# Performance work log

Hardware: AMD Instinct MI355X
Metric: run time of the kernel (lower is better)

The kernel has to match this reference:

```python
import math
import jax, jax.numpy as jnp
import numpy as np

B, HRV, WRV, CRV = 1, 32, 512, 64
CBEV, HB, WB = 128, 256, 256
D, COUT, K, HEADS, P = 128, 128, 5, 8, 6
HD = D // HEADS
NBINS = 110
RMAX, BIN = 55.0, 0.5
XMIN, XMAX, YMIN, YMAX = -55.0, 55.0, -55.0, 55.0

_ELEV = np.array([-30.67, -29.33, -28.0, -26.66, -25.33, -24.0, -22.67, -21.33,
                  -20.0, -18.67, -17.33, -16.0, -14.67, -13.33, -12.0, -10.67,
                  -9.33, -8.0, -6.66, -5.33, -4.0, -2.67, -1.33, 0.0, 1.33,
                  2.67, 4.0, 5.33, 6.67, 8.0, 9.33, 10.67], dtype=np.float32)

def _make_uvec():
    az_line = np.linspace(-math.pi, math.pi, WRV + 1, dtype=np.float32)[:-1]
    az = az_line + 0.5 * (az_line[1] - az_line[0])
    elev = np.deg2rad(_ELEV[::-1].reshape(HRV, -1).mean(axis=1)).astype(np.float32)
    az2 = np.broadcast_to(az[None, :], (HRV, WRV))
    el2 = np.broadcast_to(elev[:, None], (HRV, WRV))
    ux = np.cos(az2) * np.cos(el2)
    uy = np.sin(az2) * np.cos(el2)
    uz = np.broadcast_to(np.sin(el2), (HRV, WRV))
    return jnp.asarray(ux), jnp.asarray(uy), jnp.asarray(uz)

_UX, _UY, _UZ = _make_uvec()

def _lin(x, w, b):
    # 1x1 conv / Linear: w is torch-layout [Cout, Cin]
    return jnp.einsum('...c,oc->...o', x, w) + b

def _gn(x, gamma, beta, groups, eps=1e-5):
    Bn, H, W, C = x.shape
    xg = x.reshape(Bn, H, W, groups, C // groups)
    mu = xg.mean(axis=(1, 2, 4), keepdims=True)
    var = ((xg - mu) ** 2).mean(axis=(1, 2, 4), keepdims=True)
    xg = (xg - mu) * jax.lax.rsqrt(var + eps)
    return xg.reshape(Bn, H, W, C) * gamma + beta

def _gelu(x):
    return jax.nn.gelu(x, approximate=False)

def _conv3x3_circ(x, w):
    # torch Conv2d(3x3, padding=1, padding_mode='circular', bias=False)
    xp = jnp.pad(x, ((0, 0), (1, 1), (1, 1), (0, 0)), mode='wrap')
    k = jnp.transpose(w, (2, 3, 1, 0))  # OIHW -> HWIO
    return jax.lax.conv_general_dilated(xp, k, (1, 1), 'VALID',
                                        dimension_numbers=('NHWC', 'HWIO', 'NHWC'))

def _deform_sample(v, loc, aw):
    # v: [B, HB*WB, HEADS, HD]; loc: [B,Nq,HEADS,P,2] normalized; aw: [B,Nq,HEADS,P]
    # Emulates grid_sample(bilinear, zeros padding, align_corners=False).
    Bq = v.shape[0]
    vflat = jnp.transpose(v, (0, 2, 1, 3))       # [B, H, HW, hd]
    loc_t = jnp.transpose(loc, (0, 2, 1, 3, 4))  # [B, H, Nq, P, 2]
    aw_t = jnp.transpose(aw, (0, 2, 1, 3))       # [B, H, Nq, P]
    x = loc_t[..., 0] * WB - 0.5
    y = loc_t[..., 1] * HB - 0.5
    x0 = jnp.floor(x); y0 = jnp.floor(y)
    wx1 = x - x0; wy1 = y - y0
    x0i = x0.astype(jnp.int32); y0i = y0.astype(jnp.int32)
    gather = jax.vmap(jax.vmap(lambda vf, idx: vf[idx]))  # over B, heads
    def corner(xi, yi, wgt, acc):
        valid = (xi >= 0) & (xi < WB) & (yi >= 0) & (yi < HB)
        idx = jnp.clip(yi, 0, HB - 1) * WB + jnp.clip(xi, 0, WB - 1)
        g = gather(vflat, idx)  # [B, H, Nq, P, hd]
        return acc + g * (wgt * valid.astype(g.dtype))[..., None]
    acc = jnp.zeros(x.shape + (HD,), dtype=v.dtype)
    acc = corner(x0i,     y0i,     (1 - wx1) * (1 - wy1), acc)
    acc = corner(x0i + 1, y0i,     wx1 * (1 - wy1), acc)
    acc = corner(x0i,     y0i + 1, (1 - wx1) * wy1, acc)
    acc = corner(x0i + 1, y0i + 1, wx1 * wy1, acc)
    out = (acc * aw_t[..., None]).sum(axis=3)    # [B, H, Nq, hd]
    return jnp.transpose(out, (0, 2, 1, 3)).reshape(Bq, -1, D)

def _forward(x_rv, bev, lidar2ego_mat, wq, bq, wv, bv, wo, bo,
             qd_w1, qd_b1, qd_w2, qd_b2,
             rh_w1, rh_b1, rh_g1, rh_be1, rh_w2, rh_g2, rh_be2, rh_w3, rh_b3,
             off_w, off_b, aw_w, aw_b, vp_w, vp_b, op_w, op_b):
    Bq = x_rv.shape[0]
    Q0 = _lin(x_rv, wq, bq)                                   # [B,Hrv,Wrv,D]
    Vmap = _lin(jnp.transpose(bev, (0, 2, 3, 1)), wv, bv)     # [B,HB,WB,D]
    uvec = jnp.broadcast_to(jnp.stack([_UX, _UY, _UZ], axis=-1)[None], (Bq, HRV, WRV, 3))
    h = _gelu(_gn(_lin(jnp.concatenate([x_rv, uvec], axis=-1), rh_w1, rh_b1), rh_g1, rh_be1, 8))
    h = _gelu(_gn(_conv3x3_circ(h, rh_w2), rh_g2, rh_be2, 8))
    depth_logits = _lin(h, rh_w3, rh_b3)                      # [B,Hrv,Wrv,NBINS]
    depth_dist = jax.nn.softmax(depth_logits, axis=-1)
    topk_prob, topk_idx = jax.lax.top_k(depth_dist, K)        # [B,Hrv,Wrv,K]
    topk_depths = jnp.minimum(BIN * (topk_idx.astype(jnp.float32) + 0.5), RMAX - 0.5 * BIN)
    xl = topk_depths * _UX[None, :, :, None]
    yl = topk_depths * _UY[None, :, :, None]
    zl = topk_depths * _UZ[None, :, :, None]
    p = jnp.stack([xl, yl, zl, jnp.ones_like(xl)], axis=-1)   # [B,Hrv,Wrv,K,4]
    pe = jnp.einsum('bhwki,ij->bhwkj', p, lidar2ego_mat[0])
    rx = (pe[..., 0] - XMIN) / (XMAX - XMIN)
    ry = (pe[..., 1] - YMIN) / (YMAX - YMIN)
    ref_pts = jnp.stack([jnp.clip(rx, 0.0, 1.0), jnp.clip(ry, 0.0, 1.0)], axis=-1).reshape(Bq, -1, 2)
    qin = jnp.concatenate([jnp.broadcast_to(Q0[:, :, :, None, :], (Bq, HRV, WRV, K, D)),
                           (topk_depths / RMAX)[..., None]], axis=-1)
    query = _lin(_gelu(_lin(qin, qd_w1, qd_b1)), qd_w2, qd_b2).reshape(Bq, -1, D)
    value = Vmap.reshape(Bq, -1, D)
    # --- MSDA (mmcv MultiScaleDeformableAttention, 1 level) ---
    v = _lin(value, vp_w, vp_b).reshape(Bq, -1, HEADS, HD)
    Nq = query.shape[1]
    off = _lin(query, off_w, off_b).reshape(Bq, Nq, HEADS, P, 2)
    aw = jax.nn.softmax(_lin(query, aw_w, aw_b).reshape(Bq, Nq, HEADS, P), axis=-1)
    loc = ref_pts[:, :, None, None, :] + off / jnp.array([WB, HB], dtype=jnp.float32)
    y_msda = _lin(_deform_sample(v, loc, aw), op_w, op_b) + query  # residual add
    y_msda = y_msda.reshape(Bq, HRV, WRV, K, D)
    wgt = topk_prob / (topk_prob.sum(axis=-1, keepdims=True) + 1e-8)
    y = (y_msda * wgt[..., None]).sum(axis=3)
    y = _lin(y, wo, bo)                                       # [B,Hrv,Wrv,COUT]
    return y, jnp.transpose(depth_logits, (0, 3, 1, 2))

def setup_inputs():
    key = jax.random.key(0)
    ks = jax.random.split(key, 32)
    def rn(i, shape, s):
        return jax.random.normal(ks[i], shape, dtype=jnp.float32) * s
    return dict(
        x_rv=rn(0, (B, HRV, WRV, CRV), 1.0),
        bev=rn(1, (B, CBEV, HB, WB), 1.0),
        lidar2ego_mat=jnp.eye(4, dtype=jnp.float32)[None] + rn(2, (1, 4, 4), 0.01),
        wq=rn(3, (D, CRV), 0.05), bq=rn(4, (D,), 0.01),
        wv=rn(5, (D, CBEV), 0.05), bv=rn(6, (D,), 0.01),
        wo=rn(7, (COUT, D), 0.05), bo=rn(8, (COUT,), 0.01),
        qd_w1=rn(9, (D, D + 1), 0.05), qd_b1=rn(10, (D,), 0.01),
        qd_w2=rn(11, (D, D), 0.05), qd_b2=rn(12, (D,), 0.01),
        rh_w1=rn(13, (128, CRV + 3), 0.05), rh_b1=rn(14, (128,), 0.01),
        rh_g1=jnp.ones((128,), jnp.float32), rh_be1=jnp.zeros((128,), jnp.float32),
        rh_w2=rn(15, (64, 128, 3, 3), 0.05),
        rh_g2=jnp.ones((64,), jnp.float32), rh_be2=jnp.zeros((64,), jnp.float32),
        rh_w3=rn(16, (NBINS, 64), 0.05), rh_b3=rn(17, (NBINS,), 0.01),
        off_w=rn(18, (HEADS * P * 2, D), 0.02), off_b=rn(19, (HEADS * P * 2,), 2.0),
        aw_w=rn(20, (HEADS * P, D), 0.02), aw_b=rn(21, (HEADS * P,), 0.01),
        vp_w=rn(22, (D, D), 0.05), vp_b=rn(23, (D,), 0.01),
        op_w=rn(24, (D, D), 0.05), op_b=rn(25, (D,), 0.01),
    )

def reference(x_rv, bev, lidar2ego_mat, wq, bq, wv, bv, wo, bo,
              qd_w1, qd_b1, qd_w2, qd_b2,
              rh_w1, rh_b1, rh_g1, rh_be1, rh_w2, rh_g2, rh_be2, rh_w3, rh_b3,
              off_w, off_b, aw_w, aw_b, vp_w, vp_b, op_w, op_b):
    return _forward(x_rv, bev, lidar2ego_mat, wq, bq, wv, bv, wo, bo,
                    qd_w1, qd_b1, qd_w2, qd_b2,
                    rh_w1, rh_b1, rh_g1, rh_be1, rh_w2, rh_g2, rh_be2, rh_w3, rh_b3,
                    off_w, off_b, aw_w, aw_b, vp_w, vp_b, op_w, op_b)
```

## Files before the change

kernel.cpp:

```cpp
#include <hip/hip_runtime.h>
#include <math.h>

#define NT 256

typedef unsigned short u16;
typedef unsigned int u32;
typedef _Float16 f16;
typedef __attribute__((ext_vector_type(2))) unsigned int u32x2;
typedef __attribute__((ext_vector_type(4))) unsigned int u32x4;
typedef __attribute__((ext_vector_type(4))) float f32x4;
typedef __attribute__((ext_vector_type(8))) short s16x8;
typedef __attribute__((ext_vector_type(8))) _Float16 f16x8;

namespace {

__device__ const float c_elev[32] = {
  -30.67f,-29.33f,-28.0f,-26.66f,-25.33f,-24.0f,-22.67f,-21.33f,
  -20.0f,-18.67f,-17.33f,-16.0f,-14.67f,-13.33f,-12.0f,-10.67f,
  -9.33f,-8.0f,-6.66f,-5.33f,-4.0f,-2.67f,-1.33f,0.0f,1.33f,
  2.67f,4.0f,5.33f,6.67f,8.0f,9.33f,10.67f };

__device__ __forceinline__ float gelu_f(float x) {
  return 0.5f * x * (1.0f + erff(x * 0.70710678118654752440f));
}
__device__ __forceinline__ u16 bf16rne(float f) {
  u32 u = __builtin_bit_cast(u32, f);
  u32 r = u + 0x7FFFu + ((u >> 16) & 1u);
  return (u16)(r >> 16);
}
__device__ __forceinline__ float bf2f(u16 h) {
  u32 u = ((u32)h) << 16;
  return __builtin_bit_cast(float, u);
}
__device__ __forceinline__ float bflo(u32 v) {
  return __builtin_bit_cast(float, v << 16);
}
__device__ __forceinline__ float bfhi(u32 v) {
  return __builtin_bit_cast(float, v & 0xFFFF0000u);
}
__device__ __forceinline__ u32 packsplit(float x) {
  f16 h = (f16)x;
  f16 l = (f16)(x - (float)h);
  return (u32)__builtin_bit_cast(u16, h) | ((u32)__builtin_bit_cast(u16, l) << 16);
}
__device__ __forceinline__ void unpack16(u32x4 a, u32x4 b, f16x8& hi, f16x8& lo) {
  u32x4 h, l;
  h[0] = (a[0] & 0xFFFFu) | (a[1] << 16);  l[0] = (a[0] >> 16) | (a[1] & 0xFFFF0000u);
  h[1] = (a[2] & 0xFFFFu) | (a[3] << 16);  l[1] = (a[2] >> 16) | (a[3] & 0xFFFF0000u);
  h[2] = (b[0] & 0xFFFFu) | (b[1] << 16);  l[2] = (b[0] >> 16) | (b[1] & 0xFFFF0000u);
  h[3] = (b[2] & 0xFFFFu) | (b[3] << 16);  l[3] = (b[2] >> 16) | (b[3] & 0xFFFF0000u);
  hi = __builtin_bit_cast(f16x8, h);
  lo = __builtin_bit_cast(f16x8, l);
}

template<int COREAL, int CO, int KPAD, int CI, int PROD, int AMODE, bool DOGELU, bool OBF, bool GN = false>
__global__ __launch_bounds__(NT)
void slin(const float* __restrict__ Af, const float* __restrict__ A2,
          const u32* __restrict__ Wp, const float* __restrict__ bias,
          const float* __restrict__ gs, const float* __restrict__ gamma,
          const float* __restrict__ beta,
          float* __restrict__ outF, u16* __restrict__ outB)
{
  constexpr int BM = 64;
  constexpr int NFR = CO / 16;
  constexpr int KS = KPAD / 32;
  __shared__ u32 lds[BM * KPAD];
  const int tid = threadIdx.x;
  const long row0 = (long)blockIdx.x * BM;

  for (int i = tid; i < BM * (KPAD / 4); i += NT) {
    int r = i / (KPAD / 4), c = (i % (KPAD / 4)) * 4;
    long pix = row0 + r;
    u32x4 o;
    if constexpr (AMODE == 0) {
      if (c + 3 < CI) {
        f32x4 v = *(const f32x4*)(Af + pix * CI + c);
#pragma unroll
        for (int e = 0; e < 4; e++) {
          float x = v[e];
          if constexpr (GN) {
            int cc = c + e, g = cc >> 3;
            float mu = gs[2 * g] * (1.0f / 131072.0f);
            float var = gs[2 * g + 1] * (1.0f / 131072.0f) - mu * mu;
            x = (x - mu) * rsqrtf(var + 1e-5f) * gamma[cc] + beta[cc];
            x = gelu_f(x);
          }
          o[e] = packsplit(x);
        }
// ... 41 lines not shown
  for (int ks = 0; ks < KS; ks++) {
    const int arow = mb + lr;
    const u32 sw = (arow & 7) << 4;
    const int base = arow * KPAD * 4 + ks * 128 + kq * 32;
    u32x4 a0 = *(const u32x4*)((char*)lds + (base ^ sw));
    u32x4 a1 = *(const u32x4*)((char*)lds + ((base + 16) ^ sw));
    f16x8 ah, al;
    unpack16(a0, a1, ah, al);
#pragma unroll
    for (int nf = 0; nf < NFR; nf++) {
      const u32* wp = Wp + (nf * 16 + lr) * KPAD + ks * 32 + kq * 8;
      u32x4 w0 = *(const u32x4*)wp;
      u32x4 w1 = *(const u32x4*)(wp + 4);
      f16x8 wh, wl;
      unpack16(w0, w1, wh, wl);
      acc[nf] = __builtin_amdgcn_mfma_f32_16x16x32_f16(ah, wh, acc[nf], 0, 0, 0);
      if constexpr (PROD == 3) {
        acc[nf] = __builtin_amdgcn_mfma_f32_16x16x32_f16(ah, wl, acc[nf], 0, 0, 0);
        acc[nf] = __builtin_amdgcn_mfma_f32_16x16x32_f16(al, wh, acc[nf], 0, 0, 0);
      }
    }
  }

#pragma unroll
  for (int nf = 0; nf < NFR; nf++) {
    int col = nf * 16 + lr;
    if (col >= COREAL) continue;
    float bcol = bias[col];
#pragma unroll
    for (int r = 0; r < 4; r++) {
      long row = row0 + mb + kq * 4 + r;
      float val = acc[nf][r] + bcol;
      if constexpr (DOGELU) val = gelu_f(val);
      if constexpr (OBF) outB[row * COREAL + col] = bf16rne(val);
      else               outF[row * COREAL + col] = val;
    }
  }
}

__global__ __launch_bounds__(NT)
void conv_mfma(const float* __restrict__ X, const u32* __restrict__ Wc,
               const float* __restrict__ gs, const float* __restrict__ gamma,
               const float* __restrict__ beta, float* __restrict__ Y)
{
  __shared__ u32 lds[4 * 18 * 128];
  const int tid = threadIdx.x;
  const int bRow = (blockIdx.x >> 5) * 2;
  const int bCol = (blockIdx.x & 31) * 16;

  for (int i = tid; i < 4 * 18 * 32; i += NT) {
    int c4 = (i & 31) * 4;
    int col = (i >> 5) % 18;
    int row = i / (18 * 32);
    int gy = (bRow + row - 1 + 32) & 31;
    int gx = (bCol + col - 1 + 512) & 511;
    f32x4 v = *(const f32x4*)(X + ((long)gy * 512 + gx) * 128 + c4);
    u32x4 o;
#pragma unroll
    for (int e = 0; e < 4; e++) {
      int cc = c4 + e, g = cc >> 4;
      float mu = gs[2 * g] * (1.0f / 262144.0f);
      float var = gs[2 * g + 1] * (1.0f / 262144.0f) - mu * mu;
      float x = (v[e] - mu) * rsqrtf(var + 1e-5f) * gamma[cc] + beta[cc];
      o[e] = packsplit(gelu_f(x));
    }
    *(u32x4*)((char*)lds + ((((row * 18 + col) * 128 + c4) * 4) ^ ((col & 7) << 4))) = o;
  }
  __syncthreads();
// ... 102 lines not shown
    s16x8 af[MFR], bfr[NFR];
#pragma unroll
    for (int mf = 0; mf < MFR; mf++) {
      int r = mb + mf * 16 + lr;
      af[mf] = *(const s16x8*)(As + ((r * 256 + kof) ^ ((r & 7) << 4)));
    }
#pragma unroll
    for (int nf = 0; nf < NFR; nf++) {
      int r = nb + nf * 16 + lr;
      bfr[nf] = *(const s16x8*)(Bs + ((r * 256 + kof) ^ ((r & 7) << 4)));
    }
#pragma unroll
    for (int mf = 0; mf < MFR; mf++)
#pragma unroll
      for (int nf = 0; nf < NFR; nf++)
        acc[mf][nf] = __builtin_amdgcn_mfma_f32_16x16x32_bf16(af[mf], bfr[nf], acc[mf][nf], 0, 0, 0);
  }

#pragma unroll
  for (int mf = 0; mf < MFR; mf++) {
#pragma unroll
    for (int nf = 0; nf < NFR; nf++) {
      const int col = nb + nf * 16 + lr;
      const float bcol = bias[col];
      float ew = 0.f;
      if constexpr (DEPTH) ew = extraW[col];
#pragma unroll
      for (int r = 0; r < 4; r++) {
        long row = row0 + mb + mf * 16 + kq * 4 + r;
        float val = acc[mf][nf][r] + bcol;
        if constexpr (DEPTH) val += ew * (A2[row] * (1.0f / 55.0f));
        if constexpr (DOGELU) val = gelu_f(val);
        if constexpr (SPLIT) {
          if (col < 96) outF[row * 96 + col] = val;
          else if (col < 144) outB[row * 48 + (col - 96)] = bf16rne(val);
        } else {
          if constexpr (WF) outF[row * CO + col] = val;
          if constexpr (WBF) outB[row * CO + col] = bf16rne(val);
        }
      }
    }
  }
}

__global__ __launch_bounds__(NT)
void qmlp_kernel(const u16* __restrict__ Q0, const float* __restrict__ depths,
                 const u16* __restrict__ W1, const float* __restrict__ b1,
                 const float* __restrict__ w1last,
                 const u16* __restrict__ W2, const float* __restrict__ b2,
                 u16* __restrict__ query)
{
  __shared__ char smem[49152];
  char* As = smem;
  char* Bs = smem + 16384;
  const int tid = threadIdx.x;
  const long row0 = (long)blockIdx.x * 64;

  for (int i = tid; i < 128 * 16; i += NT) {
    int r = i >> 4, ck = i & 15;
    u32x4 v = ((const u32x4*)(W1 + r * 128))[ck];
    *(u32x4*)(Bs + ((r * 256 + ck * 16) ^ ((r & 7) << 4))) = v;
  }
  for (int i = tid; i < 64 * 16; i += NT) {
    int r = i >> 4, ck = i & 15;
    long src = (row0 + r) / 5;
    u32x4 v = ((const u32x4*)(Q0 + src * 128))[ck];
    *(u32x4*)(As + ((r * 256 + ck * 16) ^ ((r & 7) << 4))) = v;
// ... 166 lines not shown
                              const float* __restrict__ op_b, const float* __restrict__ bo,
                              u16* __restrict__ wc, float* __restrict__ bc,
                              u16* __restrict__ Wcat, float* __restrict__ cvec)
{
  int b = blockIdx.x, c = threadIdx.x;
  if (b < 128) {
    int o = b;
    float s = 0.f;
    for (int m = 0; m < 128; m++) s += vp_w[o * 128 + m] * wv[m * 128 + c];
    wc[o * 128 + c] = bf16rne(s);
    if (c == 0) {
      float bb = vp_b[o];
      for (int m = 0; m < 128; m++) bb += vp_w[o * 128 + m] * bv[m];
      bc[o] = bb;
    }
  } else {
    int o = b - 128;
    float s = 0.f;
    for (int m = 0; m < 128; m++) s += wo[o * 128 + m] * op_w[m * 128 + c];
    Wcat[o * 256 + c] = bf16rne(s);
    Wcat[o * 256 + 128 + c] = bf16rne(wo[o * 128 + c]);
    if (c == 0) {
      float bb = bo[o];
      for (int m = 0; m < 128; m++) bb += wo[o * 128 + m] * op_b[m];
      cvec[o] = bb;
    }
  }
}

__global__ void prepcvt_kernel(const float* __restrict__ qd_w1, const float* __restrict__ qd_w2,
                               const float* __restrict__ off_w, const float* __restrict__ aw_w,
                               const float* __restrict__ off_b, const float* __restrict__ aw_b,
                               const float* __restrict__ rh_w1, const float* __restrict__ rh_w3,
                               const float* __restrict__ wq, const float* __restrict__ rh_w2,
                               u16* Wq1, u16* Wq2, u16* Wmg, float* mgbias, float* w1last,
                               u32* Wh1, u32* Wlog, u32* Wq0, u32* Wcv, float* uvec)
{
  int i = blockIdx.x * NT + threadIdx.x;
  if (i < 16384) {
    int r = i >> 7, c = i & 127;
    Wq1[i] = bf16rne(qd_w1[r * 129 + c]);
    Wq2[i] = bf16rne(qd_w2[i]);
  }
  if (i < 20480) {
    int r = i >> 7, c = i & 127;
    float v = (r < 96) ? off_w[r * 128 + c] : ((r < 144) ? aw_w[(r - 96) * 128 + c] : 0.f);
    Wmg[i] = bf16rne(v);
  }
  if (i < 160) mgbias[i] = (i < 96) ? off_b[i] : ((i < 144) ? aw_b[i - 96] : 0.f);
  if (i < 128) w1last[i] = qd_w1[i * 129 + 128];
  if (i < 128 * 96) {
    int r = i / 96, c = i % 96;
    Wh1[i] = packsplit(c < 67 ? rh_w1[r * 67 + c] : 0.f);
  }
  if (i < 112 * 64) {
    int r = i / 64, c = i % 64;
    Wlog[i] = packsplit(r < 110 ? rh_w3[r * 64 + c] : 0.f);
  }
  if (i < 128 * 64) Wq0[i] = packsplit(wq[i]);
  if (i < 9 * 64 * 128) {
    int t = i / (64 * 128), o = (i / 128) % 64, c = i % 128;
    Wcv[i] = packsplit(rh_w2[(o * 128 + c) * 9 + t]);
  }
  if (i < 16384) {
    int hr = i >> 9, w = i & 511;
    float el = c_elev[31 - hr] * 0.017453292519943295f;
    float az = -3.14159265358979323846f + ((float)w + 0.5f) * (6.283185307179586477f / 512.0f);
    float ce = cosf(el);
    uvec[i * 3 + 0] = cosf(az) * ce;
    uvec[i * 3 + 1] = sinf(az) * ce;
    uvec[i * 3 + 2] = sinf(el);
  }
}

template<int C, int S>
__global__ __launch_bounds__(NT)
void gn_stats_kernel(const float* __restrict__ X, int Npix, float* __restrict__ gs)
{
  constexpr int PPB = NT / C;
  int tid = threadIdx.x;
  int c = tid % C;
  int psub = tid / C;
  float sum = 0.f, ss = 0.f;
  for (long pix = (long)blockIdx.x * PPB + psub; pix < Npix; pix += (long)gridDim.x * PPB) {
    float v = X[pix * C + c];
    sum += v; ss += v * v;
  }
  __shared__ float ls[8][2];
  if (tid < 16) ls[tid / 2][tid % 2] = 0.f;
  __syncthreads();
  int g = c / S;
  atomicAdd(&ls[g][0], sum);
  atomicAdd(&ls[g][1], ss);
  __syncthreads();
  if (tid < 16) atomicAdd(&gs[tid], ls[tid / 2][tid % 2]);
}

__global__ __launch_bounds__(NT)
void tlogits_kernel(const float* __restrict__ logits, float* __restrict__ out1)
{
  __shared__ float ls[128][111];
  int p0 = blockIdx.x * 128;
  for (int i = threadIdx.x; i < 128 * 110; i += NT) {
    int p = i / 110, c = i % 110;
    ls[p][c] = logits[(long)(p0 + p) * 110 + c];
  }
  __syncthreads();
  for (int i = threadIdx.x; i < 110 * 128; i += NT) {
    int c = i / 128, p = i % 128;
    out1[(long)c * 16384 + p0 + p] = ls[p][c];
  }
}

__global__ __launch_bounds__(NT)
void topk_kernel(const float* __restrict__ logits, float* __restrict__ depths,
                 float* __restrict__ wgt)
{
  int lane = threadIdx.x & 63;
  int pix = (blockIdx.x * NT + threadIdx.x) >> 6;
  const float* lr = logits + (long)pix * 110;
  float v0 = (lane < 110) ? lr[lane] : -1e30f;
  float v1 = (lane + 64 < 110) ? lr[lane + 64] : -1e30f;
  float m = fmaxf(v0, v1);
#pragma unroll
  for (int s = 32; s; s >>= 1) m = fmaxf(m, __shfl_xor(m, s));
  float ex = ((lane < 110) ? expf(v0 - m) : 0.f) + ((lane + 64 < 110) ? expf(v1 - m) : 0.f);
  float den = ex;
#pragma unroll
  for (int s = 32; s; s >>= 1) den += __shfl_xor(den, s);
  float pr[5]; int pi[5];
#pragma unroll
  for (int j = 0; j < 5; j++) {
    float bv; int bi;
    if (v0 >= v1) { bv = v0; bi = lane; } else { bv = v1; bi = lane + 64; }
    for (int s = 1; s < 64; s <<= 1) {
      float ov = __shfl_xor(bv, s);
      int oi = __shfl_xor(bi, s);
      if (ov > bv || (ov == bv && oi < bi)) { bv = ov; bi = oi; }
    }
    pr[j] = expf(bv - m) / den;
    pi[j] = bi;
    if (bi == lane) v0 = -1e30f;
    if (bi == lane + 64) v1 = -1e30f;
  }
  if (lane == 0) {
    float tot = pr[0] + pr[1] + pr[2] + pr[3] + pr[4] + 1e-8f;
#pragma unroll
    for (int j = 0; j < 5; j++) {
      depths[pix * 5 + j] = fminf(0.5f * ((float)pi[j] + 0.5f), 54.75f);
      wgt[pix * 5 + j] = pr[j] / tot;
    }
  }
}

__global__ __launch_bounds__(NT)
void msda_kernel(const u16* __restrict__ V, const float* __restrict__ depths,
                 const float* __restrict__ uvec, const float* __restrict__ L44,
                 const float* __restrict__ offb, const u16* __restrict__ awb,
                 u16* __restrict__ S)
{
  const int tid = threadIdx.x;
  const int kk = blockIdx.x >> 10;
  const int pg = blockIdx.x & 1023;
  const long pix = (long)pg * 16 + (tid >> 4);
  const int h = (tid >> 1) & 7;
  const int c0 = h * 16 + (tid & 1) * 8;
  const long q = pix * 5 + kk;

  float d = depths[q];
  float ux = uvec[pix * 3 + 0], uy = uvec[pix * 3 + 1], uz = uvec[pix * 3 + 2];
  float px = d * ux, py = d * uy, pz = d * uz;
  float pex = px * L44[0] + py * L44[4] + pz * L44[8] + L44[12];
  float pey = px * L44[1] + py * L44[5] + pz * L44[9] + L44[13];
  float rx = fminf(fmaxf((pex + 55.0f) * (1.0f / 110.0f), 0.f), 1.f);
  float ry = fminf(fmaxf((pey + 55.0f) * (1.0f / 110.0f), 0.f), 1.f);
  float rxs = rx * 256.0f - 0.5f;
  float rys = ry * 256.0f - 0.5f;

  const u32* ap32 = (const u32*)(awb + q * 48 + h * 6);
  u32 aw0 = ap32[0], aw1 = ap32[1], aw2 = ap32[2];
  float a[6] = { bflo(aw0), bfhi(aw0), bflo(aw1), bfhi(aw1), bflo(aw2), bfhi(aw2) };
  float mx = fmaxf(fmaxf(fmaxf(a[0], a[1]), fmaxf(a[2], a[3])), fmaxf(a[4], a[5]));
  float se = 0.f;
#pragma unroll
  for (int p = 0; p < 6; p++) { a[p] = __expf(a[p] - mx); se += a[p]; }
  const float inv = 1.0f / se;

  const f32x4* opv = (const f32x4*)(offb + q * 96 + h * 12);
  f32x4 of0 = opv[0], of1 = opv[1], of2 = opv[2];
  const float ox[6] = { of0[0], of0[2], of1[0], of1[2], of2[0], of2[2] };
  const float oy[6] = { of0[1], of0[3], of1[1], of1[3], of2[1], of2[3] };

  float acc[8];
#pragma unroll
  for (int j = 0; j < 8; j++) acc[j] = 0.f;

#pragma unroll
  for (int p = 0; p < 6; p++) {
    float x = rxs + ox[p];
    float y = rys + oy[p];
    float x0f = floorf(x), y0f = floorf(y);
    float wx = x - x0f, wy = y - y0f;
    int ix = (int)x0f, iy = (int)y0f;
    float awp = a[p] * inv;
    float wx0 = ((unsigned)ix < 256u) ? (1.f - wx) : 0.f;
    float wx1 = ((unsigned)(ix + 1) < 256u) ? wx : 0.f;
    float wy0 = ((unsigned)iy < 256u) ? (awp * (1.f - wy)) : 0.f;
    float wy1 = ((unsigned)(iy + 1) < 256u) ? (awp * wy) : 0.f;
    int xc0 = min(max(ix, 0), 255), xc1 = min(max(ix + 1, 0), 255);
    int yc0 = min(max(iy, 0), 255), yc1 = min(max(iy + 1, 0), 255);
#pragma unroll
    for (int cy = 0; cy < 2; cy++) {
      int yb = (cy ? yc1 : yc0) << 15;
      float wyv = cy ? wy1 : wy0;
#pragma unroll
      for (int cx = 0; cx < 2; cx++) {
        int idx = yb + ((cx ? xc1 : xc0) << 7) + c0;
        float m = (cx ? wx1 : wx0) * wyv;
        u32x4 v = *(const u32x4*)(V + idx);
#pragma unroll
        for (int e = 0; e < 4; e++) {
          acc[2 * e]     += m * bflo(v[e]);
          acc[2 * e + 1] += m * bfhi(v[e]);
        }
      }
    }
  }
  u32x4 o;
#pragma unroll
  for (int e = 0; e < 4; e++)
    o[e] = (u32)bf16rne(acc[2 * e]) | ((u32)bf16rne(acc[2 * e + 1]) << 16);
  *(u32x4*)(S + q * 128 + c0) = o;
}

}

extern "C" void kernel_launch(void* const* d_in, const int* in_sizes, int n_in,
                              void* d_out, int out_size, void* d_ws, size_t ws_size,
                              hipStream_t stream)
{
  (void)in_sizes; (void)n_in; (void)out_size; (void)ws_size;
  const float* x_rv   = (const float*)d_in[0];
  const float* bev    = (const float*)d_in[1];
  const float* L44    = (const float*)d_in[2];
  const float* wq     = (const float*)d_in[3];
  const float* bq     = (const float*)d_in[4];
  const float* wv     = (const float*)d_in[5];
  const float* bv     = (const float*)d_in[6];
  const float* woW    = (const float*)d_in[7];
  const float* boB    = (const float*)d_in[8];
  const float* qd_w1  = (const float*)d_in[9];
  const float* qd_b1  = (const float*)d_in[10];
  const float* qd_w2  = (const float*)d_in[11];
  const float* qd_b2  = (const float*)d_in[12];
  const float* rh_w1  = (const float*)d_in[13];
  const float* rh_b1  = (const float*)d_in[14];
  const float* rh_g1  = (const float*)d_in[15];
  const float* rh_be1 = (const float*)d_in[16];
  const float* rh_w2  = (const float*)d_in[17];
  const float* rh_g2  = (const float*)d_in[18];
  const float* rh_be2 = (const float*)d_in[19];
  const float* rh_w3  = (const float*)d_in[20];
  const float* rh_b3  = (const float*)d_in[21];
  const float* off_w  = (const float*)d_in[22];
  const float* off_b  = (const float*)d_in[23];
  const float* aw_w   = (const float*)d_in[24];
  const float* aw_b   = (const float*)d_in[25];
  const float* vp_w   = (const float*)d_in[26];
  const float* vp_b   = (const float*)d_in[27];
  const float* op_w   = (const float*)d_in[28];
  const float* op_b   = (const float*)d_in[29];

  float* outY = (float*)d_out;
  float* outL = (float*)d_out + 2097152;

  char* wsb = (char*)d_ws;
  size_t off = 0;
  auto alloc = [&](size_t bytes) -> char* {
    char* p = wsb + off;
    off += (bytes + 255) & ~(size_t)255;
    return p;
  };

  u16*   wcomb  = (u16*)alloc(32768);
  float* bcomb  = (float*)alloc(512);
  float* uvec   = (float*)alloc(196608);
  float* stats  = (float*)alloc(128);
  float* depths = (float*)alloc(327680);
  float* wgtb   = (float*)alloc(327680);
  float* w1last = (float*)alloc(512);
  u16*   Wq1    = (u16*)alloc(32768);
  u16*   Wq2    = (u16*)alloc(32768);
  u16*   Wmg    = (u16*)alloc(40960);
  float* mgbias = (float*)alloc(640);
  u16*   Wcat   = (u16*)alloc(65536);
  float* cvec   = (float*)alloc(512);
  u32*   Wh1    = (u32*)alloc(49152);
  u32*   Wlog   = (u32*)alloc(28672);
  u32*   Wq0    = (u32*)alloc(32768);
  u32*   Wcv    = (u32*)alloc(294912);
  char*  S1     = alloc(20971520);
  char*  S2     = alloc(4194304);
  char*  S3     = alloc(16777216);
  char*  S5     = alloc(20971520);
  float* offbuf = (float*)alloc(31457280);
  u16*   awbf   = (u16*)alloc(7864320);

  float* h1buf  = (float*)S1;
  float* logits = (float*)(S1 + 8388608);
  float* h2buf  = (float*)(S1 + 15597568);
  u16*   smp    = (u16*)S1;
  u16*   Q0bf   = (u16*)S2;
  u16*   vbuf   = (u16*)S3;
  u16*   querybf= (u16*)S5;

  float* stats1 = stats;
  float* stats2 = stats + 16;

  hipMemsetAsync((void*)stats, 0, 128, stream);

  prepmm_kernel<<<256, 128, 0, stream>>>(vp_w, wv, vp_b, bv, woW, op_w, op_b, boB,
                                         wcomb, bcomb, Wcat, cvec);
  prepcvt_kernel<<<288, NT, 0, stream>>>(qd_w1, qd_w2, off_w, aw_w, off_b, aw_b,
                                         rh_w1, rh_w3, wq, rh_w2,
                                         Wq1, Wq2, Wmg, mgbias, w1last,
                                         Wh1, Wlog, Wq0, Wcv, uvec);

  slin<128, 128, 64, 64, 1, 0, false, true><<<256, NT, 0, stream>>>(
      x_rv, nullptr, Wq0, bq, nullptr, nullptr, nullptr, nullptr, Q0bf);

  slin<128, 128, 96, 67, 3, 1, false, false><<<256, NT, 0, stream>>>(
      x_rv, uvec, Wh1, rh_b1, nullptr, nullptr, nullptr, h1buf, nullptr);
  gn_stats_kernel<128, 16><<<512, NT, 0, stream>>>(h1buf, 16384, stats1);
  conv_mfma<<<512, NT, 0, stream>>>(h1buf, Wcv, stats1, rh_g1, rh_be1, h2buf);
  gn_stats_kernel<64, 8><<<512, NT, 0, stream>>>(h2buf, 16384, stats2);
  slin<110, 112, 64, 64, 3, 0, false, false, true><<<256, NT, 0, stream>>>(
      h2buf, nullptr, Wlog, rh_b3, stats2, rh_g2, rh_be2, logits, nullptr);
  tlogits_kernel<<<128, NT, 0, stream>>>(logits, outL);
  topk_kernel<<<4096, NT, 0, stream>>>(logits, depths, wgtb);

  mfma_lin<128, 4, false, false, false, true, false><<<1024, NT, 0, stream>>>(
      bev, nullptr, wcomb, bcomb, nullptr, nullptr, vbuf, 65536);

  qmlp_kernel<<<1280, NT, 0, stream>>>(Q0bf, depths, Wq1, qd_b1, w1last, Wq2, qd_b2, querybf);

  mfma_lin<160, 0, false, false, false, false, true><<<1280, NT, 0, stream>>>(
      querybf, nullptr, Wmg, mgbias, nullptr, offbuf, awbf, 0);

  msda_kernel<<<5120, NT, 0, stream>>>(vbuf, depths, uvec, L44, offbuf, awbf, smp);

  outproj_kernel<<<256, NT, 0, stream>>>(smp, querybf, wgtb, Wcat, cvec, outY);
}
```

Baseline: 406.9 us.

## Store offsets as fp16, batch MSDA gathers, fuse logit transpose with top-k

The offset projection now writes sampling offsets as fp16 instead of fp32, halving that intermediate buffer, and the deformable sampler reads the packed halves. The sampler issues all 24 bilinear corner loads before accumulating, remaps block indices across 8 groups for locality, and sets a 3-blocks-per-SIMD launch bound. The logits transpose and softmax top-k are merged into one kernel that reads logits once from shared memory. The cost is fp16 rounding of offsets (offset bias is large, up to about 2), which slightly perturbs sample positions, plus higher register pressure from the batched loads.

```diff
diff --git a/kernel.cpp b/kernel.cpp
--- a/kernel.cpp
+++ b/kernel.cpp
@@ -331,7 +331,7 @@
         if constexpr (DEPTH) val += ew * (A2[row] * (1.0f / 55.0f));
         if constexpr (DOGELU) val = gelu_f(val);
         if constexpr (SPLIT) {
-          if (col < 96) outF[row * 96 + col] = val;
+          if (col < 96) ((u16*)outF)[row * 96 + col] = __builtin_bit_cast(u16, (f16)val);
           else if (col < 144) outB[row * 48 + (col - 96)] = bf16rne(val);
         } else {
           if constexpr (WF) outF[row * CO + col] = val;
@@ -629,71 +629,71 @@
 }
 
 __global__ __launch_bounds__(NT)
-void tlogits_kernel(const float* __restrict__ logits, float* __restrict__ out1)
-{
-  __shared__ float ls[128][111];
-  int p0 = blockIdx.x * 128;
-  for (int i = threadIdx.x; i < 128 * 110; i += NT) {
+void logpost_kernel(const float* __restrict__ logits, float* __restrict__ out1,
+                    float* __restrict__ depths, float* __restrict__ wgt)
+{
+  __shared__ float ls[64][112];
+  const int tid = threadIdx.x;
+  const int p0 = blockIdx.x * 64;
+  for (int i = tid; i < 64 * 110; i += NT) {
     int p = i / 110, c = i % 110;
     ls[p][c] = logits[(long)(p0 + p) * 110 + c];
   }
   __syncthreads();
-  for (int i = threadIdx.x; i < 110 * 128; i += NT) {
-    int c = i / 128, p = i % 128;
+  for (int i = tid; i < 110 * 64; i += NT) {
+    int c = i >> 6, p = i & 63;
     out1[(long)c * 16384 + p0 + p] = ls[p][c];
   }
-}
-
-__global__ __launch_bounds__(NT)
-void topk_kernel(const float* __restrict__ logits, float* __restrict__ depths,
-                 float* __restrict__ wgt)
-{
-  int lane = threadIdx.x & 63;
-  int pix = (blockIdx.x * NT + threadIdx.x) >> 6;
-  const float* lr = logits + (long)pix * 110;
-  float v0 = (lane < 110) ? lr[lane] : -1e30f;
-  float v1 = (lane + 64 < 110) ? lr[lane + 64] : -1e30f;
-  float m = fmaxf(v0, v1);
-#pragma unroll
-  for (int s = 32; s; s >>= 1) m = fmaxf(m, __shfl_xor(m, s));
-  float ex = ((lane < 110) ? expf(v0 - m) : 0.f) + ((lane + 64 < 110) ? expf(v1 - m) : 0.f);
-  float den = ex;
-#pragma unroll
-  for (int s = 32; s; s >>= 1) den += __shfl_xor(den, s);
-  float pr[5]; int pi[5];
-#pragma unroll
-  for (int j = 0; j < 5; j++) {
-    float bv; int bi;
-    if (v0 >= v1) { bv = v0; bi = lane; } else { bv = v1; bi = lane + 64; }
-    for (int s = 1; s < 64; s <<= 1) {
-      float ov = __shfl_xor(bv, s);
-      int oi = __shfl_xor(bi, s);
-      if (ov > bv || (ov == bv && oi < bi)) { bv = ov; bi = oi; }
-    }
-    pr[j] = expf(bv - m) / den;
-    pi[j] = bi;
-    if (bi == lane) v0 = -1e30f;
-    if (bi == lane + 64) v1 = -1e30f;
-  }
-  if (lane == 0) {
-    float tot = pr[0] + pr[1] + pr[2] + pr[3] + pr[4] + 1e-8f;
+  const int wave = tid >> 6, lane = tid & 63;
+  for (int t = 0; t < 16; t++) {
+    int p = wave * 16 + t;
+    float v0 = (lane < 110) ? ls[p][lane] : -1e30f;
+    float v1 = (lane + 64 < 110) ? ls[p][lane + 64] : -1e30f;
+    float m = fmaxf(v0, v1);
+#pragma unroll
+    for (int s = 32; s; s >>= 1) m = fmaxf(m, __shfl_xor(m, s));
+    float ex = ((lane < 110) ? expf(v0 - m) : 0.f) + ((lane + 64 < 110) ? expf(v1 - m) : 0.f);
+    float den = ex;
+#pragma unroll
+    for (int s = 32; s; s >>= 1) den += __shfl_xor(den, s);
+    float pr[5]; int pi[5];
 #pragma unroll
     for (int j = 0; j < 5; j++) {
-      depths[pix * 5 + j] = fminf(0.5f * ((float)pi[j] + 0.5f), 54.75f);
-      wgt[pix * 5 + j] = pr[j] / tot;
-    }
-  }
-}
-
-__global__ __launch_bounds__(NT)
+      float bv; int bi;
+      if (v0 >= v1) { bv = v0; bi = lane; } else { bv = v1; bi = lane + 64; }
+      for (int s = 1; s < 64; s <<= 1) {
+        float ov = __shfl_xor(bv, s);
+        int oi = __shfl_xor(bi, s);
+        if (ov > bv || (ov == bv && oi < bi)) { bv = ov; bi = oi; }
+      }
+      pr[j] = expf(bv - m) / den;
+      pi[j] = bi;
+      if (bi == lane) v0 = -1e30f;
+      if (bi == lane + 64) v1 = -1e30f;
+    }
+    if (lane == 0) {
+      long pix = p0 + p;
+      float tot = pr[0] + pr[1] + pr[2] + pr[3] + pr[4] + 1e-8f;
+#pragma unroll
+      for (int j = 0; j < 5; j++) {
+        depths[pix * 5 + j] = fminf(0.5f * ((float)pi[j] + 0.5f), 54.75f);
+        wgt[pix * 5 + j] = pr[j] / tot;
+      }
+    }
+  }
+}
+
+__global__ __launch_bounds__(NT, 3)
 void msda_kernel(const u16* __restrict__ V, const float* __restrict__ depths,
                  const float* __restrict__ uvec, const float* __restrict__ L44,
-                 const float* __restrict__ offb, const u16* __restrict__ awb,
+                 const u16* __restrict__ offH, const u16* __restrict__ awb,
                  u16* __restrict__ S)
 {
   const int tid = threadIdx.x;
-  const int kk = blockIdx.x >> 10;
-  const int pg = blockIdx.x & 1023;
+  const int hw = blockIdx.x;
+  const int bid = (hw & 7) * 640 + (hw >> 3);
+  const int kk = bid >> 10;
+  const int pg = bid & 1023;
   const long pix = (long)pg * 16 + (tid >> 4);
   const int h = (tid >> 1) & 7;
   const int c0 = h * 16 + (tid & 1) * 8;
@@ -718,19 +718,19 @@
   for (int p = 0; p < 6; p++) { a[p] = __expf(a[p] - mx); se += a[p]; }
   const float inv = 1.0f / se;
 
-  const f32x4* opv = (const f32x4*)(offb + q * 96 + h * 12);
-  f32x4 of0 = opv[0], of1 = opv[1], of2 = opv[2];
-  const float ox[6] = { of0[0], of0[2], of1[0], of1[2], of2[0], of2[2] };
-  const float oy[6] = { of0[1], of0[3], of1[1], of1[3], of2[1], of2[3] };
-
-  float acc[8];
-#pragma unroll
-  for (int j = 0; j < 8; j++) acc[j] = 0.f;
-
+  const u32* op16 = (const u32*)(offH + q * 96 + h * 12);
+  u32x2 o01 = *(const u32x2*)op16;
+  u32x2 o23 = *(const u32x2*)(op16 + 2);
+  u32x2 o45 = *(const u32x2*)(op16 + 4);
+  u32 ou[6] = { o01[0], o01[1], o23[0], o23[1], o45[0], o45[1] };
+
+  int ad[6][4]; float wt[6][4];
 #pragma unroll
   for (int p = 0; p < 6; p++) {
-    float x = rxs + ox[p];
-    float y = rys + oy[p];
+    float ox = (float)__builtin_bit_cast(f16, (u16)(ou[p] & 0xFFFFu));
+    float oy = (float)__builtin_bit_cast(f16, (u16)(ou[p] >> 16));
+    float x = rxs + ox;
+    float y = rys + oy;
     float x0f = floorf(x), y0f = floorf(y);
     float wx = x - x0f, wy = y - y0f;
     int ix = (int)x0f, iy = (int)y0f;
@@ -741,23 +741,31 @@
     float wy1 = ((unsigned)(iy + 1) < 256u) ? (awp * wy) : 0.f;
     int xc0 = min(max(ix, 0), 255), xc1 = min(max(ix + 1, 0), 255);
     int yc0 = min(max(iy, 0), 255), yc1 = min(max(iy + 1, 0), 255);
-#pragma unroll
-    for (int cy = 0; cy < 2; cy++) {
-      int yb = (cy ? yc1 : yc0) << 15;
-      float wyv = cy ? wy1 : wy0;
-#pragma unroll
-      for (int cx = 0; cx < 2; cx++) {
-        int idx = yb + ((cx ? xc1 : xc0) << 7) + c0;
-        float m = (cx ? wx1 : wx0) * wyv;
-        u32x4 v = *(const u32x4*)(V + idx);
-#pragma unroll
-        for (int e = 0; e < 4; e++) {
-          acc[2 * e]     += m * bflo(v[e]);
-          acc[2 * e + 1] += m * bfhi(v[e]);
-        }
-      }
-    }
-  }
+    ad[p][0] = (yc0 << 15) + (xc0 << 7) + c0;  wt[p][0] = wx0 * wy0;
+    ad[p][1] = (yc0 << 15) + (xc1 << 7) + c0;  wt[p][1] = wx1 * wy0;
+    ad[p][2] = (yc1 << 15) + (xc0 << 7) + c0;  wt[p][2] = wx0 * wy1;
+    ad[p][3] = (yc1 << 15) + (xc1 << 7) + c0;  wt[p][3] = wx1 * wy1;
+  }
+  u32x4 vv[6][4];
+#pragma unroll
+  for (int p = 0; p < 6; p++)
+#pragma unroll
+    for (int c = 0; c < 4; c++)
+      vv[p][c] = *(const u32x4*)(V + ad[p][c]);
+  float acc[8];
+#pragma unroll
+  for (int j = 0; j < 8; j++) acc[j] = 0.f;
+#pragma unroll
+  for (int p = 0; p < 6; p++)
+#pragma unroll
+    for (int c = 0; c < 4; c++) {
+      float m = wt[p][c];
+#pragma unroll
+      for (int e = 0; e < 4; e++) {
+        acc[2 * e]     += m * bflo(vv[p][c][e]);
+        acc[2 * e + 1] += m * bfhi(vv[p][c][e]);
+      }
+    }
   u32x4 o;
 #pragma unroll
   for (int e = 0; e < 4; e++)
@@ -835,7 +843,7 @@
   char*  S2     = alloc(4194304);
   char*  S3     = alloc(16777216);
   char*  S5     = alloc(20971520);
-  float* offbuf = (float*)alloc(31457280);
+  u16*   offH   = (u16*)alloc(15728640);
   u16*   awbf   = (u16*)alloc(7864320);
 
   float* h1buf  = (float*)S1;
@@ -868,8 +876,7 @@
   gn_stats_kernel<64, 8><<<512, NT, 0, stream>>>(h2buf, 16384, stats2);
   slin<110, 112, 64, 64, 3, 0, false, false, true><<<256, NT, 0, stream>>>(
       h2buf, nullptr, Wlog, rh_b3, stats2, rh_g2, rh_be2, logits, nullptr);
-  tlogits_kernel<<<128, NT, 0, stream>>>(logits, outL);
-  topk_kernel<<<4096, NT, 0, stream>>>(logits, depths, wgtb);
+  logpost_kernel<<<256, NT, 0, stream>>>(logits, outL, depths, wgtb);
 
   mfma_lin<128, 4, false, false, false, true, false><<<1024, NT, 0, stream>>>(
       bev, nullptr, wcomb, bcomb, nullptr, nullptr, vbuf, 65536);
@@ -877,9 +884,9 @@
   qmlp_kernel<<<1280, NT, 0, stream>>>(Q0bf, depths, Wq1, qd_b1, w1last, Wq2, qd_b2, querybf);
 
   mfma_lin<160, 0, false, false, false, false, true><<<1280, NT, 0, stream>>>(
-      querybf, nullptr, Wmg, mgbias, nullptr, offbuf, awbf, 0);
-
-  msda_kernel<<<5120, NT, 0, stream>>>(vbuf, depths, uvec, L44, offbuf, awbf, smp);
+      querybf, nullptr, Wmg, mgbias, nullptr, (float*)offH, awbf, 0);
+
+  msda_kernel<<<5120, NT, 0, stream>>>(vbuf, depths, uvec, L44, offH, awbf, smp);
 
   outproj_kernel<<<256, NT, 0, stream>>>(smp, querybf, wgtb, Wcat, cvec, outY);
 }
```

New measurement: 480.3 us. 18.0% more time.

## Merge Q0 and head linear, store offsets in fp16, two queries per msda thread

Applied to the files above, without the earlier changes.

Combines the query projection and the range-head first linear into one slin launch with a concatenated 256-wide weight and a split epilogue, so x_rv is read once and one launch is dropped. Sampling offsets are now written as fp16 rather than fp32, halving that intermediate's traffic. The msda kernel processes two pixels per thread, with half the blocks and more loads in flight per thread. The cost is fp16 offset precision and higher register pressure in msda. The merged slin reuses the AMODE=1 path with uvec inputs, so the Q0 rows also see the extra padded columns, which are zeroed in the weights.

```diff
diff --git a/kernel.cpp b/kernel.cpp
--- a/kernel.cpp
+++ b/kernel.cpp
@@ -53,7 +53,8 @@
   lo = __builtin_bit_cast(f16x8, l);
 }
 
-template<int COREAL, int CO, int KPAD, int CI, int PROD, int AMODE, bool DOGELU, bool OBF, bool GN = false>
+template<int COREAL, int CO, int KPAD, int CI, int PROD, int AMODE, bool DOGELU, bool OBF,
+         bool GN = false, bool MERGEQ = false>
 __global__ __launch_bounds__(NT)
 void slin(const float* __restrict__ Af, const float* __restrict__ A2,
           const u32* __restrict__ Wp, const float* __restrict__ bias,
@@ -161,8 +162,14 @@
       long row = row0 + mb + kq * 4 + r;
       float val = acc[nf][r] + bcol;
       if constexpr (DOGELU) val = gelu_f(val);
-      if constexpr (OBF) outB[row * COREAL + col] = bf16rne(val);
-      else               outF[row * COREAL + col] = val;
+      if constexpr (MERGEQ) {
+        if (col < 128) outF[row * 128 + col] = val;
+        else           outB[row * 128 + (col - 128)] = bf16rne(val);
+      } else if constexpr (OBF) {
+        outB[row * COREAL + col] = bf16rne(val);
+      } else {
+        outF[row * COREAL + col] = val;
+      }
     }
   }
 }
@@ -331,7 +338,7 @@
         if constexpr (DEPTH) val += ew * (A2[row] * (1.0f / 55.0f));
         if constexpr (DOGELU) val = gelu_f(val);
         if constexpr (SPLIT) {
-          if (col < 96) outF[row * 96 + col] = val;
+          if (col < 96) ((u16*)outF)[row * 96 + col] = __builtin_bit_cast(u16, (f16)val);
           else if (col < 144) outB[row * 48 + (col - 96)] = bf16rne(val);
         } else {
           if constexpr (WF) outF[row * CO + col] = val;
@@ -564,9 +571,10 @@
                                const float* __restrict__ off_w, const float* __restrict__ aw_w,
                                const float* __restrict__ off_b, const float* __restrict__ aw_b,
                                const float* __restrict__ rh_w1, const float* __restrict__ rh_w3,
-                               const float* __restrict__ wq, const float* __restrict__ rh_w2,
+                               const float* __restrict__ wq, const float* __restrict__ bq,
+                               const float* __restrict__ rh_b1, const float* __restrict__ rh_w2,
                                u16* Wq1, u16* Wq2, u16* Wmg, float* mgbias, float* w1last,
-                               u32* Wh1, u32* Wlog, u32* Wq0, u32* Wcv, float* uvec)
+                               u32* Wmrg, float* biasMrg, u32* Wlog, u32* Wcv, float* uvec)
 {
   int i = blockIdx.x * NT + threadIdx.x;
   if (i < 16384) {
@@ -581,15 +589,18 @@
   }
   if (i < 160) mgbias[i] = (i < 96) ? off_b[i] : ((i < 144) ? aw_b[i - 96] : 0.f);
   if (i < 128) w1last[i] = qd_w1[i * 129 + 128];
-  if (i < 128 * 96) {
+  if (i < 24576) {
     int r = i / 96, c = i % 96;
-    Wh1[i] = packsplit(c < 67 ? rh_w1[r * 67 + c] : 0.f);
-  }
+    float v;
+    if (r < 128) v = (c < 67) ? rh_w1[r * 67 + c] : 0.f;
+    else         v = (c < 64) ? wq[(r - 128) * 64 + c] : 0.f;
+    Wmrg[i] = packsplit(v);
+  }
+  if (i < 256) biasMrg[i] = (i < 128) ? rh_b1[i] : bq[i - 128];
   if (i < 112 * 64) {
     int r = i / 64, c = i % 64;
     Wlog[i] = packsplit(r < 110 ? rh_w3[r * 64 + c] : 0.f);
   }
-  if (i < 128 * 64) Wq0[i] = packsplit(wq[i]);
   if (i < 9 * 64 * 128) {
     int t = i / (64 * 128), o = (i / 128) % 64, c = i % 128;
     Wcv[i] = packsplit(rh_w2[(o * 128 + c) * 9 + t]);
@@ -685,20 +696,12 @@
   }
 }
 
-__global__ __launch_bounds__(NT)
-void msda_kernel(const u16* __restrict__ V, const float* __restrict__ depths,
-                 const float* __restrict__ uvec, const float* __restrict__ L44,
-                 const float* __restrict__ offb, const u16* __restrict__ awb,
-                 u16* __restrict__ S)
-{
-  const int tid = threadIdx.x;
-  const int kk = blockIdx.x >> 10;
-  const int pg = blockIdx.x & 1023;
-  const long pix = (long)pg * 16 + (tid >> 4);
-  const int h = (tid >> 1) & 7;
-  const int c0 = h * 16 + (tid & 1) * 8;
-  const long q = pix * 5 + kk;
-
+__device__ __forceinline__ void msda_setup(
+    const float* __restrict__ depths, const float* __restrict__ uvec,
+    const float* __restrict__ L44, const u16* __restrict__ offH,
+    const u16* __restrict__ awb, long pix, long q, int h,
+    float& rxs, float& rys, float a[6], u32 ou[6])
+{
   float d = depths[q];
   float ux = uvec[pix * 3 + 0], uy = uvec[pix * 3 + 1], uz = uvec[pix * 3 + 2];
   float px = d * ux, py = d * uy, pz = d * uz;
@@ -706,63 +709,114 @@
   float pey = px * L44[1] + py * L44[5] + pz * L44[9] + L44[13];
   float rx = fminf(fmaxf((pex + 55.0f) * (1.0f / 110.0f), 0.f), 1.f);
   float ry = fminf(fmaxf((pey + 55.0f) * (1.0f / 110.0f), 0.f), 1.f);
-  float rxs = rx * 256.0f - 0.5f;
-  float rys = ry * 256.0f - 0.5f;
-
+  rxs = rx * 256.0f - 0.5f;
+  rys = ry * 256.0f - 0.5f;
   const u32* ap32 = (const u32*)(awb + q * 48 + h * 6);
   u32 aw0 = ap32[0], aw1 = ap32[1], aw2 = ap32[2];
-  float a[6] = { bflo(aw0), bfhi(aw0), bflo(aw1), bfhi(aw1), bflo(aw2), bfhi(aw2) };
+  a[0] = bflo(aw0); a[1] = bfhi(aw0); a[2] = bflo(aw1);
+  a[3] = bfhi(aw1); a[4] = bflo(aw2); a[5] = bfhi(aw2);
   float mx = fmaxf(fmaxf(fmaxf(a[0], a[1]), fmaxf(a[2], a[3])), fmaxf(a[4], a[5]));
   float se = 0.f;
 #pragma unroll
   for (int p = 0; p < 6; p++) { a[p] = __expf(a[p] - mx); se += a[p]; }
-  const float inv = 1.0f / se;
-
-  const f32x4* opv = (const f32x4*)(offb + q * 96 + h * 12);
-  f32x4 of0 = opv[0], of1 = opv[1], of2 = opv[2];
-  const float ox[6] = { of0[0], of0[2], of1[0], of1[2], of2[0], of2[2] };
-  const float oy[6] = { of0[1], of0[3], of1[1], of1[3], of2[1], of2[3] };
-
-  float acc[8];
-#pragma unroll
-  for (int j = 0; j < 8; j++) acc[j] = 0.f;
+  float inv = 1.0f / se;
+#pragma unroll
+  for (int p = 0; p < 6; p++) a[p] *= inv;
+  const u32* op16 = (const u32*)(offH + q * 96 + h * 12);
+#pragma unroll
+  for (int p = 0; p < 6; p++) ou[p] = op16[p];
+}
+
+__device__ __forceinline__ void msda_corners(float rxs, float rys, u32 oup, float ap, int c0,
+                                             int ad[4], float wt[4])
+{
+  float ox = (float)__builtin_bit_cast(f16, (u16)(oup & 0xFFFFu));
+  float oy = (float)__builtin_bit_cast(f16, (u16)(oup >> 16));
+  float x = rxs + ox, y = rys + oy;
+  float x0f = floorf(x), y0f = floorf(y);
+  float wx = x - x0f, wy = y - y0f;
+  int ix = (int)x0f, iy = (int)y0f;
+  float wx0 = ((unsigned)ix < 256u) ? (1.f - wx) : 0.f;
+  float wx1 = ((unsigned)(ix + 1) < 256u) ? wx : 0.f;
+  float wy0 = ((unsigned)iy < 256u) ? (ap * (1.f - wy)) : 0.f;
+  float wy1 = ((unsigned)(iy + 1) < 256u) ? (ap * wy) : 0.f;
+  int xc0 = min(max(ix, 0), 255), xc1 = min(max(ix + 1, 0), 255);
+  int yc0 = min(max(iy, 0), 255), yc1 = min(max(iy + 1, 0), 255);
+  ad[0] = (yc0 << 15) + (xc0 << 7) + c0;  wt[0] = wx0 * wy0;
+  ad[1] = (yc0 << 15) + (xc1 << 7) + c0;  wt[1] = wx1 * wy0;
+  ad[2] = (yc1 << 15) + (xc0 << 7) + c0;  wt[2] = wx0 * wy1;
+  ad[3] = (yc1 << 15) + (xc1 << 7) + c0;  wt[3] = wx1 * wy1;
+}
+
+__global__ __launch_bounds__(NT)
+void msda_kernel(const u16* __restrict__ V, const float* __restrict__ depths,
+                 const float* __restrict__ uvec, const float* __restrict__ L44,
+                 const u16* __restrict__ offH, const u16* __restrict__ awb,
+                 u16* __restrict__ S)
+{
+  const int tid = threadIdx.x;
+  const int bid = blockIdx.x;
+  const int kk = bid >> 9;
+  const int pg = bid & 511;
+  const long pixA = (long)pg * 32 + (tid >> 4);
+  const long pixB = pixA + 16;
+  const int h = (tid >> 1) & 7;
+  const int c0 = h * 16 + (tid & 1) * 8;
+  const long qA = pixA * 5 + kk;
+  const long qB = pixB * 5 + kk;
+
+  float rxsA, rysA, rxsB, rysB;
+  float aA[6], aB[6];
+  u32 ouA[6], ouB[6];
+  msda_setup(depths, uvec, L44, offH, awb, pixA, qA, h, rxsA, rysA, aA, ouA);
+  msda_setup(depths, uvec, L44, offH, awb, pixB, qB, h, rxsB, rysB, aB, ouB);
+
+  float accA[8], accB[8];
+#pragma unroll
+  for (int j = 0; j < 8; j++) { accA[j] = 0.f; accB[j] = 0.f; }
 
 #pragma unroll
   for (int p = 0; p < 6; p++) {
-    float x = rxs + ox[p];
-    float y = rys + oy[p];
-    float x0f = floorf(x), y0f = floorf(y);
-    float wx = x - x0f, wy = y - y0f;
-    int ix = (int)x0f, iy = (int)y0f;
-    float awp = a[p] * inv;
-    float wx0 = ((unsigned)ix < 256u) ? (1.f - wx) : 0.f;
-    float wx1 = ((unsigned)(ix + 1) < 256u) ? wx : 0.f;
-    float wy0 = ((unsigned)iy < 256u) ? (awp * (1.f - wy)) : 0.f;
-    float wy1 = ((unsigned)(iy + 1) < 256u) ? (awp * wy) : 0.f;
-    int xc0 = min(max(ix, 0), 255), xc1 = min(max(ix + 1, 0), 255);
-    int yc0 = min(max(iy, 0), 255), yc1 = min(max(iy + 1, 0), 255);
-#pragma unroll
-    for (int cy = 0; cy < 2; cy++) {
-      int yb = (cy ? yc1 : yc0) << 15;
-      float wyv = cy ? wy1 : wy0;
-#pragma unroll
-      for (int cx = 0; cx < 2; cx++) {
-        int idx = yb + ((cx ? xc1 : xc0) << 7) + c0;
-        float m = (cx ? wx1 : wx0) * wyv;
-        u32x4 v = *(const u32x4*)(V + idx);
-#pragma unroll
-        for (int e = 0; e < 4; e++) {
-          acc[2 * e]     += m * bflo(v[e]);
-          acc[2 * e + 1] += m * bfhi(v[e]);
-        }
-      }
-    }
-  }
-  u32x4 o;
-#pragma unroll
-  for (int e = 0; e < 4; e++)
-    o[e] = (u32)bf16rne(acc[2 * e]) | ((u32)bf16rne(acc[2 * e + 1]) << 16);
-  *(u32x4*)(S + q * 128 + c0) = o;
+    int adA[4], adB[4];
+    float wtA[4], wtB[4];
+    msda_corners(rxsA, rysA, ouA[p], aA[p], c0, adA, wtA);
+    msda_corners(rxsB, rysB, ouB[p], aB[p], c0, adB, wtB);
+    u32x2 vA0 = *(const u32x2*)(V + adA[0]);
+    u32x2 vA0h = *(const u32x2*)(V + adA[0] + 4);
+    u32x2 vA1 = *(const u32x2*)(V + adA[1]);
+    u32x2 vA1h = *(const u32x2*)(V + adA[1] + 4);
+    u32x2 vA2 = *(const u32x2*)(V + adA[2]);
+    u32x2 vA2h = *(const u32x2*)(V + adA[2] + 4);
+    u32x2 vA3 = *(const u32x2*)(V + adA[3]);
+    u32x2 vA3h = *(const u32x2*)(V + adA[3] + 4);
+    u32x2 vB0 = *(const u32x2*)(V + adB[0]);
+    u32x2 vB0h = *(const u32x2*)(V + adB[0] + 4);
+    u32x2 vB1 = *(const u32x2*)(V + adB[1]);
+    u32x2 vB1h = *(const u32x2*)(V + adB[1] + 4);
+    u32x2 vB2 = *(const u32x2*)(V + adB[2]);
+    u32x2 vB2h = *(const u32x2*)(V + adB[2] + 4);
+    u32x2 vB3 = *(const u32x2*)(V + adB[3]);
+    u32x2 vB3h = *(const u32x2*)(V + adB[3] + 4);
+#pragma unroll
+    for (int e = 0; e < 2; e++) {
+      accA[e * 2]     += wtA[0] * bflo(vA0[e]) + wtA[1] * bflo(vA1[e]) + wtA[2] * bflo(vA2[e]) + wtA[3] * bflo(vA3[e]);
+      accA[e * 2 + 1] += wtA[0] * bfhi(vA0[e]) + wtA[1] * bfhi(vA1[e]) + wtA[2] * bfhi(vA2[e]) + wtA[3] * bfhi(vA3[e]);
+      accA[4 + e * 2]     += wtA[0] * bflo(vA0h[e]) + wtA[1] * bflo(vA1h[e]) + wtA[2] * bflo(vA2h[e]) + wtA[3] * bflo(vA3h[e]);
+      accA[4 + e * 2 + 1] += wtA[0] * bfhi(vA0h[e]) + wtA[1] * bfhi(vA1h[e]) + wtA[2] * bfhi(vA2h[e]) + wtA[3] * bfhi(vA3h[e]);
+      accB[e * 2]     += wtB[0] * bflo(vB0[e]) + wtB[1] * bflo(vB1[e]) + wtB[2] * bflo(vB2[e]) + wtB[3] * bflo(vB3[e]);
+      accB[e * 2 + 1] += wtB[0] * bfhi(vB0[e]) + wtB[1] * bfhi(vB1[e]) + wtB[2] * bfhi(vB2[e]) + wtB[3] * bfhi(vB3[e]);
+      accB[4 + e * 2]     += wtB[0] * bflo(vB0h[e]) + wtB[1] * bflo(vB1h[e]) + wtB[2] * bflo(vB2h[e]) + wtB[3] * bflo(vB3h[e]);
+      accB[4 + e * 2 + 1] += wtB[0] * bfhi(vB0h[e]) + wtB[1] * bfhi(vB1h[e]) + wtB[2] * bfhi(vB2h[e]) + wtB[3] * bfhi(vB3h[e]);
+    }
+  }
+  u32x4 oA, oB;
+#pragma unroll
+  for (int e = 0; e < 4; e++) {
+    oA[e] = (u32)bf16rne(accA[2 * e]) | ((u32)bf16rne(accA[2 * e + 1]) << 16);
+    oB[e] = (u32)bf16rne(accB[2 * e]) | ((u32)bf16rne(accB[2 * e + 1]) << 16);
+  }
+  *(u32x4*)(S + qA * 128 + c0) = oA;
+  *(u32x4*)(S + qB * 128 + c0) = oB;
 }
 
 }
@@ -827,15 +881,15 @@
   float* mgbias = (float*)alloc(640);
   u16*   Wcat   = (u16*)alloc(65536);
   float* cvec   = (float*)alloc(512);
-  u32*   Wh1    = (u32*)alloc(49152);
+  u32*   Wmrg   = (u32*)alloc(98304);
+  float* biasMrg= (float*)alloc(1024);
   u32*   Wlog   = (u32*)alloc(28672);
-  u32*   Wq0    = (u32*)alloc(32768);
   u32*   Wcv    = (u32*)alloc(294912);
   char*  S1     = alloc(20971520);
   char*  S2     = alloc(4194304);
   char*  S3     = alloc(16777216);
   char*  S5     = alloc(20971520);
-  float* offbuf = (float*)alloc(31457280);
+  u16*   offH   = (u16*)alloc(15728640);
   u16*   awbf   = (u16*)alloc(7864320);
 
   float* h1buf  = (float*)S1;
@@ -854,15 +908,13 @@
   prepmm_kernel<<<256, 128, 0, stream>>>(vp_w, wv, vp_b, bv, woW, op_w, op_b, boB,
                                          wcomb, bcomb, Wcat, cvec);
   prepcvt_kernel<<<288, NT, 0, stream>>>(qd_w1, qd_w2, off_w, aw_w, off_b, aw_b,
-                                         rh_w1, rh_w3, wq, rh_w2,
+                                         rh_w1, rh_w3, wq, bq, rh_b1, rh_w2,
                                          Wq1, Wq2, Wmg, mgbias, w1last,
-                                         Wh1, Wlog, Wq0, Wcv, uvec);
-
-  slin<128, 128, 64, 64, 1, 0, false, true><<<256, NT, 0, stream>>>(
-      x_rv, nullptr, Wq0, bq, nullptr, nullptr, nullptr, nullptr, Q0bf);
-
-  slin<128, 128, 96, 67, 3, 1, false, false><<<256, NT, 0, stream>>>(
-      x_rv, uvec, Wh1, rh_b1, nullptr, nullptr, nullptr, h1buf, nullptr);
+                                         Wmrg, biasMrg, Wlog, Wcv, uvec);
+
+  slin<256, 256, 96, 67, 3, 1, false, false, false, true><<<256, NT, 0, stream>>>(
+      x_rv, uvec, Wmrg, biasMrg, nullptr, nullptr, nullptr, h1buf, Q0bf);
+
   gn_stats_kernel<128, 16><<<512, NT, 0, stream>>>(h1buf, 16384, stats1);
   conv_mfma<<<512, NT, 0, stream>>>(h1buf, Wcv, stats1, rh_g1, rh_be1, h2buf);
   gn_stats_kernel<64, 8><<<512, NT, 0, stream>>>(h2buf, 16384, stats2);
@@ -877,9 +929,9 @@
   qmlp_kernel<<<1280, NT, 0, stream>>>(Q0bf, depths, Wq1, qd_b1, w1last, Wq2, qd_b2, querybf);
 
   mfma_lin<160, 0, false, false, false, false, true><<<1280, NT, 0, stream>>>(
-      querybf, nullptr, Wmg, mgbias, nullptr, offbuf, awbf, 0);
-
-  msda_kernel<<<5120, NT, 0, stream>>>(vbuf, depths, uvec, L44, offbuf, awbf, smp);
+      querybf, nullptr, Wmg, mgbias, nullptr, (float*)offH, awbf, 0);
+
+  msda_kernel<<<2560, NT, 0, stream>>>(vbuf, depths, uvec, L44, offH, awbf, smp);
 
   outproj_kernel<<<256, NT, 0, stream>>>(smp, querybf, wgtb, Wcat, cvec, outY);
 }
```

Result: slower. 429.3 us (+5.5%).
